# Kernel optimization log

Measured on AMD Instinct MI355X. Metric: run time of the kernel, lower is better.

Reference implementation:

```python
import jax, jax.numpy as jnp
import numpy as np

# ---- DMP constants (from DMPParameters with N=5, tau=1, dt=1/(T*l), Dof=9, a_z=25) ----
N_BASIS = 5
T_STEPS = 10
L_SUB = 10
DIM = 9                      # len(state_index)
TAU = 1.0
DT = TAU / (T_STEPS * L_SUB)            # 0.01
TIME_STEPS = int(round(TAU / DT)) + 1   # 101
A_X = 1.0
A_Z = 25.0
B_Z = A_Z / 4.0
_c_np = np.exp(-A_X * np.linspace(0.0, 1.0, N_BASIS))
C = jnp.asarray(_c_np, dtype=jnp.float32)                          # rbf centers
H = jnp.asarray(N_BASIS ** 1.5 / _c_np / A_X, dtype=jnp.float32)   # rbf widths (sigma2)


def _integrate(w, y0, dy0, goal):
    """Euler integration of the DMP dynamical system.
    w: (R, N) basis weights; y0, dy0, goal: (R,) with R = batch*DIM.
    Returns Y: (R, TIME_STEPS) positions."""
    scale = goal - y0  # fixed forcing-term scaling

    def step(carry, _):
        y, z, x = carry
        x = x + (-A_X * x / TAU) * DT                  # canonical system
        psi = jnp.exp(-H * (x - C) ** 2)               # (N,) gaussian rbf
        fx = (w @ psi) * x * scale / jnp.sum(psi)      # (R,) forcing term
        dz = (A_Z * (B_Z * (goal - y) - z) + fx) / TAU
        dy = z / TAU
        y = y + dy * DT
        z = z + dz * DT
        return (y, z, x), y

    z0 = dy0 * TAU
    _, ys = jax.lax.scan(step, (y0, z0, jnp.float32(1.0)), None, length=TIME_STEPS - 1)
    # prepend initial position, transpose to (R, TIME_STEPS)
    return jnp.concatenate([y0[None, :], ys], axis=0).T


def setup_inputs():
    key = jax.random.key(0)
    ks = jax.random.split(key, 4)
    B, D_IN, HID = 16384, 128, 2048
    out_size = DIM * (N_BASIS + 1)  # 54 = N*dim + dim
    return {
        "input": jax.random.normal(ks[0], (B, D_IN), jnp.float32),
        "W0": jax.random.normal(ks[1], (HID, D_IN), jnp.float32) / np.sqrt(D_IN),
        "b0": jnp.full((HID,), 0.1, jnp.float32),
        "W1": jax.random.normal(ks[2], (HID, HID), jnp.float32) / np.sqrt(HID),
        "b1": jnp.full((HID,), 0.1, jnp.float32),
        "Wl": jax.random.normal(ks[3], (out_size, HID), jnp.float32) / np.sqrt(HID),
        "bl": jnp.zeros((out_size,), jnp.float32),
    }


def reference(input, W0, b0, W1, b1, Wl, bl):
    B = input.shape[0]
    # MLP backbone with tanh hidden activation
    h = jnp.tanh(input @ W0.T + b0)
    h = jnp.tanh(h @ W1.T + b1)
    out = (h @ Wl.T + bl) * 100.0                          # (B, DIM*(N+1))
    # split DMP parameters: goal then basis weights
    goal = out[:, :DIM].reshape(-1)                        # (B*DIM,)
    w = out[:, DIM:DIM * (N_BASIS + 1)].reshape(-1, N_BASIS)  # (B*DIM, N)
    y0 = input[:, 7:16].reshape(-1)                        # state_index
    dy0 = input[:, 22:31].reshape(-1)                      # vel_index
    Y = _integrate(w, y0, dy0, goal)                       # (B*DIM, 101)
    y = Y.reshape(B, DIM, TIME_STEPS)[:, :, ::L_SUB]       # (B, DIM, T+1)
    return y[:, :, 1:] - y[:, :, :-1]                      # (B, DIM, T)
```

## Files before the change

### kernel.cpp

```cpp
#include <hip/hip_runtime.h>
#include <hip/hip_fp16.h>
#include <math.h>

typedef _Float16 f16;
typedef _Float16 f16x8 __attribute__((ext_vector_type(8)));
typedef _Float16 f16x4v __attribute__((ext_vector_type(4)));
typedef float f32x4 __attribute__((ext_vector_type(4)));

#define B_SZ 16384
#define D_INP 128
#define HID 2048
#define DIMS 9
#define OUTC 54
#define OUTP 64
#define NZ3 4

__device__ __forceinline__ void load_lds16(const f16* g, f16* l) {
    __builtin_amdgcn_global_load_lds(
        (__attribute__((address_space(1))) void*)(g),
        (__attribute__((address_space(3))) void*)(l),
        16, 0, 0);
}

__device__ __forceinline__ float fast_tanh(float x) {
    float e = __builtin_amdgcn_exp2f(2.885390081777927f * x);
    return 1.0f - 2.0f * __builtin_amdgcn_rcpf(e + 1.0f);
}

#define N4_W0  (HID * D_INP / 4)
#define N4_W1  (HID * HID / 4)
#define N4_WL  (OUTP * HID / 4)
__global__ __launch_bounds__(256) void cvt_fused_kernel(
    const float* __restrict__ W0, const float* __restrict__ W1,
    const float* __restrict__ Wl,
    f16* __restrict__ w0q, f16* __restrict__ w1q, f16* __restrict__ wlq)
{
    int i = blockIdx.x * 256 + threadIdx.x;
    const float* s; f16* d; int j;
    if (i < N4_W0) { s = W0; d = w0q; j = i; }
    else if (i < N4_W0 + N4_W1) { s = W1; d = w1q; j = i - N4_W0; }
    else {
        j = i - N4_W0 - N4_W1;
        int e0 = j * 4, row = e0 >> 11, col = e0 & (HID - 1);
        f16x4v o;
        if (row < OUTC) {
            float4 v = ((const float4*)Wl)[(row * HID + col) >> 2];
            o.x = (f16)v.x; o.y = (f16)v.y; o.z = (f16)v.z; o.w = (f16)v.w;
        } else {
            o.x = (f16)0.f; o.y = (f16)0.f; o.z = (f16)0.f; o.w = (f16)0.f;
        }
        ((f16x4v*)wlq)[j] = o;
        return;
    }
    float4 v = ((const float4*)s)[j];
    f16x4v o;
    o.x = (f16)v.x; o.y = (f16)v.y; o.z = (f16)v.z; o.w = (f16)v.w;
    ((f16x4v*)d)[j] = o;
}

template <int BN, int EPI>
__global__ __launch_bounds__(256, 2) void gemm_nt(
    const f16* __restrict__ A, const f16* __restrict__ Bm,
    const float* __restrict__ bias, void* __restrict__ Cout,
    int M, int N, int K, int bias_n)
{
    constexpr int BM = 128, BK = 64;
    constexpr int NI = BN / 32;
    __shared__ __align__(16) f16 sa[BM * BK];
    __shared__ __align__(16) f16 sb[BN * BK];

    const int tid  = threadIdx.x;
    const int lane = tid & 63;
    const int wave = tid >> 6;
    const int wm = wave >> 1, wn = wave & 1;

    const int flat = blockIdx.x + blockIdx.y * gridDim.x;
    const int gsz  = 8 * gridDim.y;
    const int grp  = flat / gsz;
    const int rem  = flat - grp * gsz;
    const int m0 = (grp * 8 + (rem & 7)) * BM;
    const int n0 = (rem >> 3) * BN;

    const int k_len = K / gridDim.z;
    const int k_beg = blockIdx.z * k_len;
    const int k_end = k_beg + k_len;

    f32x4 acc[4][NI];
    #pragma unroll
    for (int i = 0; i < 4; ++i)
        #pragma unroll
        for (int j = 0; j < NI; ++j) acc[i][j] = (f32x4){0.f, 0.f, 0.f, 0.f};

    const int r8 = lane >> 3;
    const int cg = (((lane & 7) ^ r8) << 3);

    for (int k0 = k_beg; k0 < k_end; k0 += BK) {
        #pragma unroll
        for (int c = 0; c < (BM * BK * 2) / 4096; ++c) {
            int o = c * 4096 + wave * 1024;
            const f16* gp = A + (size_t)(m0 + (o >> 7) + r8) * K + k0 + cg;
            load_lds16(gp, (f16*)((char*)sa + o));
        }
        #pragma unroll
        for (int c = 0; c < (BN * BK * 2) / 4096; ++c) {
            int o = c * 4096 + wave * 1024;
            const f16* gp = Bm + (size_t)(n0 + (o >> 7) + r8) * K + k0 + cg;
            load_lds16(gp, (f16*)((char*)sb + o));
        }
        __syncthreads();

        #pragma unroll
        for (int kc = 0; kc < 2; ++kc) {
            f16x8 af[4], bf[NI];
            #pragma unroll
            for (int mi = 0; mi < 4; ++mi) {
                int ar = wm * 64 + mi * 16 + (lane & 15);
                af[mi] = *(const f16x8*)&sa[ar * 64 + ((((kc << 2) | (lane >> 4)) ^ (ar & 7)) << 3)];
            }
            #pragma unroll
            for (int ni = 0; ni < NI; ++ni) {
                int br = wn * (BN / 2) + ni * 16 + (lane & 15);
                bf[ni] = *(const f16x8*)&sb[br * 64 + ((((kc << 2) | (lane >> 4)) ^ (br & 7)) << 3)];
            }
            #pragma unroll
            for (int mi = 0; mi < 4; ++mi)
                #pragma unroll
                for (int ni = 0; ni < NI; ++ni)
                    acc[mi][ni] = __builtin_amdgcn_mfma_f32_16x16x32_f16(af[mi], bf[ni], acc[mi][ni], 0, 0, 0);
        }
        __syncthreads();
    }

    const int crow0 = m0 + wm * 64 + (lane >> 4) * 4;
    const int ccol0 = n0 + wn * (BN / 2) + (lane & 15);
    if (EPI == 0) {
        f16* C = (f16*)Cout;
        #pragma unroll
        for (int mi = 0; mi < 4; ++mi)
            #pragma unroll
            for (int ni = 0; ni < NI; ++ni) {
                int col = ccol0 + ni * 16;
                float bv = bias[col];
                #pragma unroll
                for (int r2 = 0; r2 < 4; ++r2) {
                    float v = fast_tanh(acc[mi][ni][r2] + bv);
                    C[(size_t)(crow0 + mi * 16 + r2) * N + col] = (f16)v;
                }
            }
    } else {
        float* C = (float*)Cout + (size_t)blockIdx.z * M * N;
        #pragma unroll
        for (int mi = 0; mi < 4; ++mi)
            #pragma unroll
            for (int ni = 0; ni < NI; ++ni) {
                int col = ccol0 + ni * 16;
                float bv = (blockIdx.z == 0 && col < bias_n) ? bias[col] * 100.0f : 0.0f;
                #pragma unroll
                for (int r2 = 0; r2 < 4; ++r2) {
                    float v = acc[mi][ni][r2] * 100.0f + bv;
                    C[(size_t)(crow0 + mi * 16 + r2) * N + col] = v;
                }
            }
    }
}

__global__ __launch_bounds__(256, 2) void gemm1_f32a(
    const float* __restrict__ A, const f16* __restrict__ Bm,
    const float* __restrict__ bias, f16* __restrict__ C)
{
    constexpr int BM = 128, BK = 64, BN = 128, NI = 4;
    constexpr int N = HID, K = D_INP;
    __shared__ __align__(16) f16 sa[BM * BK];
    __shared__ __align__(16) f16 sb[BN * BK];

    const int tid  = threadIdx.x;
    const int lane = tid & 63;
    const int wave = tid >> 6;
    const int wm = wave >> 1, wn = wave & 1;

    const int flat = blockIdx.x + blockIdx.y * gridDim.x;
    const int gsz  = 8 * gridDim.y;
    const int grp  = flat / gsz;
    const int rem  = flat - grp * gsz;
    const int m0 = (grp * 8 + (rem & 7)) * BM;
    const int n0 = (rem >> 3) * BN;

    f32x4 acc[4][NI];
    #pragma unroll
    for (int i = 0; i < 4; ++i)
        #pragma unroll
        for (int j = 0; j < NI; ++j) acc[i][j] = (f32x4){0.f, 0.f, 0.f, 0.f};

    const int r8 = lane >> 3;
    const int cg = (((lane & 7) ^ r8) << 3);

    for (int k0 = 0; k0 < K; k0 += BK) {
        #pragma unroll
        for (int c = 0; c < (BM * BK * 2) / 4096; ++c) {
            int o = c * 4096 + wave * 1024;
            const float* gp = A + (size_t)(m0 + (o >> 7) + r8) * K + k0 + cg;
            float4 v0 = *(const float4*)gp;
            float4 v1 = *(const float4*)(gp + 4);
            f16x8 h;
            h[0] = (f16)v0.x; h[1] = (f16)v0.y; h[2] = (f16)v0.z; h[3] = (f16)v0.w;
            h[4] = (f16)v1.x; h[5] = (f16)v1.y; h[6] = (f16)v1.z; h[7] = (f16)v1.w;
            *(f16x8*)((char*)sa + o + (lane << 4)) = h;
        }
        #pragma unroll
        for (int c = 0; c < (BN * BK * 2) / 4096; ++c) {
            int o = c * 4096 + wave * 1024;
            const f16* gp = Bm + (size_t)(n0 + (o >> 7) + r8) * K + k0 + cg;
            load_lds16(gp, (f16*)((char*)sb + o));
        }
        __syncthreads();

        #pragma unroll
        for (int kc = 0; kc < 2; ++kc) {
            f16x8 af[4], bf[NI];
            #pragma unroll
            for (int mi = 0; mi < 4; ++mi) {
                int ar = wm * 64 + mi * 16 + (lane & 15);
                af[mi] = *(const f16x8*)&sa[ar * 64 + ((((kc << 2) | (lane >> 4)) ^ (ar & 7)) << 3)];
            }
            #pragma unroll
            for (int ni = 0; ni < NI; ++ni) {
                int br = wn * 64 + ni * 16 + (lane & 15);
                bf[ni] = *(const f16x8*)&sb[br * 64 + ((((kc << 2) | (lane >> 4)) ^ (br & 7)) << 3)];
            }
            #pragma unroll
            for (int mi = 0; mi < 4; ++mi)
                #pragma unroll
                for (int ni = 0; ni < NI; ++ni)
                    acc[mi][ni] = __builtin_amdgcn_mfma_f32_16x16x32_f16(af[mi], bf[ni], acc[mi][ni], 0, 0, 0);
        }
        __syncthreads();
    }

    const int crow0 = m0 + wm * 64 + (lane >> 4) * 4;
    const int ccol0 = n0 + wn * 64 + (lane & 15);
    #pragma unroll
    for (int mi = 0; mi < 4; ++mi)
        #pragma unroll
        for (int ni = 0; ni < NI; ++ni) {
            int col = ccol0 + ni * 16;
            float bv = bias[col];
            #pragma unroll
            for (int r2 = 0; r2 < 4; ++r2) {
                float v = fast_tanh(acc[mi][ni][r2] + bv);
                C[(size_t)(crow0 + mi * 16 + r2) * N + col] = (f16)v;
            }
        }
}

__global__ __launch_bounds__(256) void integrate_kernel(
    const float* __restrict__ out3p, const float* __restrict__ input,
    float* __restrict__ out)
{
    __shared__ float g[500];
    {
        int k = threadIdx.x;
        if (k < 100) {
            float x = expf(-0.010050335853501441f * (float)(k + 1));
            float psi[5], ssum = 0.0f;
            #pragma unroll
            for (int n = 0; n < 5; ++n) {
                float c = expf(-0.25f * (float)n);
                float h = 11.180339887498949f / c;
                float dx = x - c;
                psi[n] = expf(-h * dx * dx);
                ssum += psi[n];
            }
            float inv = x / ssum;
            #pragma unroll
            for (int n = 0; n < 5; ++n) g[k * 5 + n] = psi[n] * inv;
        }
    }
    __syncthreads();

    int r = blockIdx.x * 256 + threadIdx.x;
    int b = r / DIMS, d = r - b * DIMS;

    float goal = 0.f, w0 = 0.f, w1 = 0.f, w2 = 0.f, w3 = 0.f, w4 = 0.f;
    #pragma unroll
    for (int z = 0; z < NZ3; ++z) {
        const float* ob = out3p + (size_t)z * B_SZ * OUTP + (size_t)b * OUTP;
        goal += ob[d];
        w0 += ob[DIMS + d * 5 + 0];
        w1 += ob[DIMS + d * 5 + 1];
        w2 += ob[DIMS + d * 5 + 2];
        w3 += ob[DIMS + d * 5 + 3];
        w4 += ob[DIMS + d * 5 + 4];
    }

    float y = input[(size_t)b * D_INP + 7 + d];
    float z = input[(size_t)b * D_INP + 22 + d];
    const float scale = goal - y;

    float prev = y;
    float* op = out + (size_t)b * (DIMS * 10) + d * 10;
    int j = 0;
    for (int k = 0; k < 100; ++k) {
        const float* gk = &g[k * 5];
        float fx = scale * (w0 * gk[0] + w1 * gk[1] + w2 * gk[2] + w3 * gk[3] + w4 * gk[4]);
        float dz = 25.0f * (6.25f * (goal - y) - z) + fx;
        y = y + z * 0.01f;
        z = z + dz * 0.01f;
        if ((k % 10) == 9) { op[j] = y - prev; prev = y; ++j; }
    }
}

extern "C" void kernel_launch(void* const* d_in, const int* in_sizes, int n_in,
                              void* d_out, int out_size, void* d_ws, size_t ws_size,
                              hipStream_t stream) {
    (void)in_sizes; (void)n_in; (void)out_size; (void)ws_size;
    const float* input = (const float*)d_in[0];
    const float* W0 = (const float*)d_in[1];
    const float* b0 = (const float*)d_in[2];
    const float* W1 = (const float*)d_in[3];
    const float* b1 = (const float*)d_in[4];
    const float* Wl = (const float*)d_in[5];
    const float* bl = (const float*)d_in[6];
    float* out = (float*)d_out;

    f16* w0q = (f16*)d_ws;
    f16* w1q = w0q + (size_t)HID * D_INP;
    f16* wlq = w1q + (size_t)HID * HID;
    f16* h1  = wlq + (size_t)OUTP * HID;
    f16* h2  = h1 + (size_t)B_SZ * HID;
    float* out3p = (float*)h1;

    int n4_total = N4_W0 + N4_W1 + N4_WL;
    cvt_fused_kernel<<<(n4_total + 255) / 256, 256, 0, stream>>>(
        W0, W1, Wl, w0q, w1q, wlq);

    gemm1_f32a<<<dim3(B_SZ / 128, HID / 128), 256, 0, stream>>>(
        input, w0q, b0, h1);
    gemm_nt<128, 0><<<dim3(B_SZ / 128, HID / 128, 1), 256, 0, stream>>>(
        h1, w1q, b1, (void*)h2, B_SZ, HID, HID, HID);
    gemm_nt<64, 1><<<dim3(B_SZ / 128, 1, NZ3), 256, 0, stream>>>(
        h2, wlq, bl, (void*)out3p, B_SZ, OUTP, HID, OUTC);

    integrate_kernel<<<B_SZ * DIMS / 256, 256, 0, stream>>>(out3p, input, out);
}
```

Measured before the change: 268.6 us.

## Replace hidden-layer GEMM with 256x256 8-phase pipelined MFMA kernel

```diff
diff --git a/kernel.cpp b/kernel.cpp
--- a/kernel.cpp
+++ b/kernel.cpp
@@ -164,6 +164,171 @@
     }
 }
 
+#define G2_K 2048
+#define G2_N 2048
+
+__global__ __launch_bounds__(512, 2) void gemm2_8ph(
+    const f16* __restrict__ A, const f16* __restrict__ Bm,
+    const float* __restrict__ bias, f16* __restrict__ C)
+{
+    constexpr int K = G2_K, N = G2_N;
+    constexpr int NT = K / 64;
+    __shared__ __align__(16) f16 sa[2][256 * 64];
+    __shared__ __align__(16) f16 sb[2][256 * 64];
+
+    const int tid  = threadIdx.x;
+    const int lane = tid & 63;
+    const int wave = tid >> 6;
+    const int wm   = wave >> 2;
+    const int wn   = wave & 3;
+    const int l15  = lane & 15;
+    const int l4   = lane >> 4;
+    const int r8   = lane >> 3;
+    const int cg   = (((lane & 7) ^ r8) << 3);
+
+    const int flat = blockIdx.x;
+    const int wgid = (flat & 7) * 64 + (flat >> 3);
+    const int m0 = (wgid >> 3) * 256;
+    const int n0 = (wgid & 7) * 256;
+
+    const f16* aSt = A  + (size_t)(m0 + wave * 8 + r8) * K + cg;
+    const f16* bSt = Bm + (size_t)(n0 + wave * 8 + r8) * K + cg;
+
+    f32x4 acc[8][4];
+    #pragma unroll
+    for (int i = 0; i < 8; ++i)
+        #pragma unroll
+        for (int j = 0; j < 4; ++j) acc[i][j] = (f32x4){0.f, 0.f, 0.f, 0.f};
+
+    f16x8 af0[4], af1[4], bf0[4], bf1[4];
+
+#define STAGE_A(bufi, tile, h) { \
+    load_lds16(aSt + (size_t)((h) * 128) * K + (tile) * 64, \
+               (f16*)((char*)sa[bufi] + (h) * 16384 + wave * 1024)); \
+    load_lds16(aSt + (size_t)((h) * 128 + 64) * K + (tile) * 64, \
+               (f16*)((char*)sa[bufi] + (h) * 16384 + 8192 + wave * 1024)); }
+#define STAGE_B(bufi, tile, h) { \
+    load_lds16(bSt + (size_t)((h) * 128) * K + (tile) * 64, \
+               (f16*)((char*)sb[bufi] + (h) * 16384 + wave * 1024)); \
+    load_lds16(bSt + (size_t)((h) * 128 + 64) * K + (tile) * 64, \
+               (f16*)((char*)sb[bufi] + (h) * 16384 + 8192 + wave * 1024)); }
+#define LDA4(dst, bufi, kc, mh) { \
+    _Pragma("unroll") \
+    for (int mi = 0; mi < 4; ++mi) { \
+        int ar = wm * 128 + (mh) * 64 + mi * 16 + l15; \
+        dst[mi] = *(const f16x8*)&sa[bufi][ar * 64 + (((((kc) << 2) | l4) ^ (ar & 7)) << 3)]; \
+    } }
+#define LDB4(dst, bufi, kc) { \
+    _Pragma("unroll") \
+    for (int ni = 0; ni < 4; ++ni) { \
+        int br = wn * 64 + ni * 16 + l15; \
+        dst[ni] = *(const f16x8*)&sb[bufi][br * 64 + (((((kc) << 2) | l4) ^ (br & 7)) << 3)]; \
+    } }
+#define MFMA16(aset, bset, mh) { \
+    _Pragma("unroll") \
+    for (int mi = 0; mi < 4; ++mi) \
+        _Pragma("unroll") \
+        for (int ni = 0; ni < 4; ++ni) \
+            acc[(mh) * 4 + mi][ni] = __builtin_amdgcn_mfma_f32_16x16x32_f16( \
+                aset[mi], bset[ni], acc[(mh) * 4 + mi][ni], 0, 0, 0); }
+#define BAR   __builtin_amdgcn_s_barrier()
+#define WLG   { asm volatile("s_waitcnt lgkmcnt(0)" ::: "memory"); \
+                __builtin_amdgcn_sched_barrier(0); }
+#define WVM4  asm volatile("s_waitcnt vmcnt(4)" ::: "memory")
+#define WVM0  asm volatile("s_waitcnt vmcnt(0)" ::: "memory")
+#define PRIO1 __builtin_amdgcn_s_setprio(1)
+#define PRIO0 __builtin_amdgcn_s_setprio(0)
+
+    STAGE_A(0, 0, 0); STAGE_A(0, 0, 1);
+    STAGE_B(0, 0, 0); STAGE_B(0, 0, 1);
+    STAGE_B(1, 1, 0); STAGE_B(1, 1, 1);
+    WVM4;
+    BAR;
+
+    #pragma unroll 1
+    for (int j = 0; j < NT / 2 - 1; ++j) {
+        const int t = 2 * j;
+        LDA4(af0, 0, 0, 0); LDB4(bf0, 0, 0);
+        STAGE_A(1, t + 1, 0);
+        BAR; WLG; PRIO1; MFMA16(af0, bf0, 0); PRIO0; BAR;
+        LDA4(af1, 0, 0, 1); LDB4(bf1, 0, 1);
+        STAGE_A(1, t + 1, 1);
+        BAR; WLG; PRIO1; MFMA16(af1, bf0, 1); PRIO0; BAR;
+        LDA4(af0, 0, 1, 0);
+        STAGE_B(0, t + 2, 0);
+        BAR; WLG; PRIO1; MFMA16(af0, bf1, 0); PRIO0; BAR;
+        LDA4(af1, 0, 1, 1);
+        STAGE_B(0, t + 2, 1);
+        BAR; WLG; PRIO1; MFMA16(af1, bf1, 1); PRIO0; WVM4; BAR;
+        LDA4(af0, 1, 0, 0); LDB4(bf0, 1, 0);
+        STAGE_A(0, t + 2, 0);
+        BAR; WLG; PRIO1; MFMA16(af0, bf0, 0); PRIO0; BAR;
+        LDA4(af1, 1, 0, 1); LDB4(bf1, 1, 1);
+        STAGE_A(0, t + 2, 1);
+        BAR; WLG; PRIO1; MFMA16(af1, bf0, 1); PRIO0; BAR;
+        LDA4(af0, 1, 1, 0);
+        STAGE_B(1, t + 3, 0);
+        BAR; WLG; PRIO1; MFMA16(af0, bf1, 0); PRIO0; BAR;
+        LDA4(af1, 1, 1, 1);
+        STAGE_B(1, t + 3, 1);
+        BAR; WLG; PRIO1; MFMA16(af1, bf1, 1); PRIO0; WVM4; BAR;
+    }
+    {
+        LDA4(af0, 0, 0, 0); LDB4(bf0, 0, 0);
+        STAGE_A(1, NT - 1, 0);
+        BAR; WLG; PRIO1; MFMA16(af0, bf0, 0); PRIO0; BAR;
+
+        LDA4(af1, 0, 0, 1); LDB4(bf1, 0, 1);
+        STAGE_A(1, NT - 1, 1);
+        BAR; WLG; PRIO1; MFMA16(af1, bf0, 1); PRIO0; BAR;
+
+        LDA4(af0, 0, 1, 0);
+        BAR; WLG; PRIO1; MFMA16(af0, bf1, 0); PRIO0; BAR;
+
+        LDA4(af1, 0, 1, 1);
+        BAR; WLG; PRIO1; MFMA16(af1, bf1, 1); PRIO0; WVM0; BAR;
+
+        LDA4(af0, 1, 0, 0); LDB4(bf0, 1, 0);
+        BAR; WLG; PRIO1; MFMA16(af0, bf0, 0); PRIO0; BAR;
+
+        LDA4(af1, 1, 0, 1); LDB4(bf1, 1, 1);
+        BAR; WLG; PRIO1; MFMA16(af1, bf0, 1); PRIO0; BAR;
+
+        LDA4(af0, 1, 1, 0);
+        BAR; WLG; PRIO1; MFMA16(af0, bf1, 0); PRIO0; BAR;
+
+        LDA4(af1, 1, 1, 1);
+        BAR; WLG; PRIO1; MFMA16(af1, bf1, 1); PRIO0; BAR;
+    }
+
+#undef STAGE_A
+#undef STAGE_B
+#undef LDA4
+#undef LDB4
+#undef MFMA16
+#undef BAR
+#undef WLG
+#undef WVM4
+#undef WVM0
+#undef PRIO1
+#undef PRIO0
+
+    const int crow0 = m0 + wm * 128 + l4 * 4;
+    const int ccol0 = n0 + wn * 64 + l15;
+    #pragma unroll
+    for (int mi = 0; mi < 8; ++mi)
+        #pragma unroll
+        for (int ni = 0; ni < 4; ++ni) {
+            int col = ccol0 + ni * 16;
+            float bv = bias[col];
+            #pragma unroll
+            for (int r2 = 0; r2 < 4; ++r2) {
+                float v = fast_tanh(acc[mi][ni][r2] + bv);
+                C[(size_t)(crow0 + mi * 16 + r2) * N + col] = (f16)v;
+            }
+        }
+}
+
 __global__ __launch_bounds__(256, 2) void gemm1_f32a(
     const float* __restrict__ A, const f16* __restrict__ Bm,
     const float* __restrict__ bias, f16* __restrict__ C)
@@ -335,8 +500,8 @@
 
     gemm1_f32a<<<dim3(B_SZ / 128, HID / 128), 256, 0, stream>>>(
         input, w0q, b0, h1);
-    gemm_nt<128, 0><<<dim3(B_SZ / 128, HID / 128, 1), 256, 0, stream>>>(
-        h1, w1q, b1, (void*)h2, B_SZ, HID, HID, HID);
+    gemm2_8ph<<<dim3((B_SZ / 256) * (HID / 256)), 512, 0, stream>>>(
+        h1, w1q, b1, h2);
     gemm_nt<64, 1><<<dim3(B_SZ / 128, 1, NZ3), 256, 0, stream>>>(
         h2, wlq, bl, (void*)out3p, B_SZ, OUTP, HID, OUTC);
 
```

New measurement: 277.7 us. 3.4% more time.

## Double-buffer LDS in the hidden-layer GEMM to overlap loads with MFMA

Applied to the files above, without the earlier changes.

```diff
diff --git a/kernel.cpp b/kernel.cpp
--- a/kernel.cpp
+++ b/kernel.cpp
@@ -164,6 +164,110 @@
     }
 }
 
+__global__ __launch_bounds__(256, 2) void gemm2_db(
+    const f16* __restrict__ A, const f16* __restrict__ Bm,
+    const float* __restrict__ bias, f16* __restrict__ C)
+{
+    constexpr int BM = 128, BK = 64, BN = 128, NI = 4;
+    constexpr int N = HID, K = HID;
+    constexpr int NT = K / BK;
+    __shared__ __align__(16) f16 sa0[BM * BK];
+    __shared__ __align__(16) f16 sa1[BM * BK];
+    __shared__ __align__(16) f16 sb0[BN * BK];
+    __shared__ __align__(16) f16 sb1[BN * BK];
+
+    const int tid  = threadIdx.x;
+    const int lane = tid & 63;
+    const int wave = tid >> 6;
+    const int wm = wave >> 1, wn = wave & 1;
+
+    const int flat = blockIdx.x + blockIdx.y * gridDim.x;
+    const int gsz  = 8 * gridDim.y;
+    const int grp  = flat / gsz;
+    const int rem  = flat - grp * gsz;
+    const int m0 = (grp * 8 + (rem & 7)) * BM;
+    const int n0 = (rem >> 3) * BN;
+
+    f32x4 acc[4][NI];
+    #pragma unroll
+    for (int i = 0; i < 4; ++i)
+        #pragma unroll
+        for (int j = 0; j < NI; ++j) acc[i][j] = (f32x4){0.f, 0.f, 0.f, 0.f};
+
+    const int r8 = lane >> 3;
+    const int cg = (((lane & 7) ^ r8) << 3);
+
+#define G2_STAGE(k0, sap, sbp) { \
+    _Pragma("unroll") \
+    for (int c = 0; c < (BM * BK * 2) / 4096; ++c) { \
+        int o = c * 4096 + wave * 1024; \
+        load_lds16(A + (size_t)(m0 + (o >> 7) + r8) * K + (k0) + cg, \
+                   (f16*)((char*)(sap) + o)); \
+    } \
+    _Pragma("unroll") \
+    for (int c = 0; c < (BN * BK * 2) / 4096; ++c) { \
+        int o = c * 4096 + wave * 1024; \
+        load_lds16(Bm + (size_t)(n0 + (o >> 7) + r8) * K + (k0) + cg, \
+                   (f16*)((char*)(sbp) + o)); \
+    } }
+
+#define G2_COMPUTE(sap, sbp) { \
+    _Pragma("unroll") \
+    for (int kc = 0; kc < 2; ++kc) { \
+        f16x8 af[4], bf[NI]; \
+        _Pragma("unroll") \
+        for (int mi = 0; mi < 4; ++mi) { \
+            int ar = wm * 64 + mi * 16 + (lane & 15); \
+            af[mi] = *(const f16x8*)&(sap)[ar * 64 + ((((kc << 2) | (lane >> 4)) ^ (ar & 7)) << 3)]; \
+        } \
+        _Pragma("unroll") \
+        for (int ni = 0; ni < NI; ++ni) { \
+            int br = wn * 64 + ni * 16 + (lane & 15); \
+            bf[ni] = *(const f16x8*)&(sbp)[br * 64 + ((((kc << 2) | (lane >> 4)) ^ (br & 7)) << 3)]; \
+        } \
+        _Pragma("unroll") \
+        for (int mi = 0; mi < 4; ++mi) \
+            _Pragma("unroll") \
+            for (int ni = 0; ni < NI; ++ni) \
+                acc[mi][ni] = __builtin_amdgcn_mfma_f32_16x16x32_f16(af[mi], bf[ni], acc[mi][ni], 0, 0, 0); \
+    } }
+
+    G2_STAGE(0, sa0, sb0);
+    __syncthreads();
+
+    #pragma unroll 1
+    for (int t = 0; t < NT - 2; t += 2) {
+        G2_STAGE((t + 1) * BK, sa1, sb1);
+        G2_COMPUTE(sa0, sb0);
+        __syncthreads();
+        G2_STAGE((t + 2) * BK, sa0, sb0);
+        G2_COMPUTE(sa1, sb1);
+        __syncthreads();
+    }
+    G2_STAGE((NT - 1) * BK, sa1, sb1);
+    G2_COMPUTE(sa0, sb0);
+    __syncthreads();
+    G2_COMPUTE(sa1, sb1);
+
+#undef G2_STAGE
+#undef G2_COMPUTE
+
+    const int crow0 = m0 + wm * 64 + (lane >> 4) * 4;
+    const int ccol0 = n0 + wn * 64 + (lane & 15);
+    #pragma unroll
+    for (int mi = 0; mi < 4; ++mi)
+        #pragma unroll
+        for (int ni = 0; ni < NI; ++ni) {
+            int col = ccol0 + ni * 16;
+            float bv = bias[col];
+            #pragma unroll
+            for (int r2 = 0; r2 < 4; ++r2) {
+                float v = fast_tanh(acc[mi][ni][r2] + bv);
+                C[(size_t)(crow0 + mi * 16 + r2) * N + col] = (f16)v;
+            }
+        }
+}
+
 __global__ __launch_bounds__(256, 2) void gemm1_f32a(
     const float* __restrict__ A, const f16* __restrict__ Bm,
     const float* __restrict__ bias, f16* __restrict__ C)
@@ -335,8 +439,8 @@
 
     gemm1_f32a<<<dim3(B_SZ / 128, HID / 128), 256, 0, stream>>>(
         input, w0q, b0, h1);
-    gemm_nt<128, 0><<<dim3(B_SZ / 128, HID / 128, 1), 256, 0, stream>>>(
-        h1, w1q, b1, (void*)h2, B_SZ, HID, HID, HID);
+    gemm2_db<<<dim3(B_SZ / 128, HID / 128), 256, 0, stream>>>(
+        h1, w1q, b1, h2);
     gemm_nt<64, 1><<<dim3(B_SZ / 128, 1, NZ3), 256, 0, stream>>>(
         h2, wlq, bl, (void*)out3p, B_SZ, OUTP, HID, OUTC);
 
```

After: 271.3 us. Within noise of the previous version (+1.0%).
